# Optimization experiments

Hardware: AMD Instinct MI355X
Metric: run time of the kernel (lower is better)

## Reference

```python
import jax, jax.numpy as jnp
import numpy as np

DIM = 768
HEADS = 16
DIM_HEAD = DIM // HEADS
SCALE = DIM_HEAD ** -0.5


def setup_inputs() -> dict:
    key = jax.random.key(0)
    k1, k2, k3, k4 = jax.random.split(key, 4)
    B, N = 8, 1024
    x = jax.random.normal(k1, (B, N, DIM), dtype=jnp.float32)
    # nn.Linear(dim, 3*dim, bias=False): stored so that qkv = x @ Wqkv
    Wqkv = jax.random.normal(k2, (DIM, 3 * DIM), dtype=jnp.float32) * (DIM ** -0.5)
    Wo = jax.random.normal(k3, (DIM, DIM), dtype=jnp.float32) * (DIM ** -0.5)
    bo = jax.random.normal(k4, (DIM,), dtype=jnp.float32) * 0.01
    return {"x": x, "Wqkv": Wqkv, "Wo": Wo, "bo": bo}


def reference(x, Wqkv, Wo, bo):
    B, N, _ = x.shape
    qkv = x @ Wqkv                                   # [B, N, 3*dim]
    # Faithful to torch: qkv.view(3, B, h, N, dim_head) — raw memory reshape
    qkv = jnp.reshape(qkv, (3, B, HEADS, N, DIM_HEAD))
    q, k, v = qkv[0], qkv[1], qkv[2]                 # each [B, h, N, dh]
    attn = jnp.einsum('bhnd,bhmd->bhnm', q, k) * SCALE   # [B, h, N, N]
    weight = jax.nn.softmax(attn, axis=-1)
    context = jnp.einsum('bhnm,bhmd->bhnd', weight, v)   # [B, h, N, dh]
    # Faithful to torch: context.view(B, -1, dim) — raw memory reshape
    concat = jnp.reshape(context, (B, N, DIM))
    return concat @ Wo + bo                          # dropout is identity at eval
```

## Files before the change

### kernel.cpp

```cpp
#include <hip/hip_runtime.h>
#include <hip/hip_bf16.h>

typedef __bf16 bf16x8 __attribute__((ext_vector_type(8)));
typedef __bf16 bf16x4 __attribute__((ext_vector_type(4)));
typedef float  f32x4  __attribute__((ext_vector_type(4)));

#define C2LOG 0.20823509f

__device__ __forceinline__ void gload_lds16(const __bf16* g, __bf16* l) {
    __builtin_amdgcn_global_load_lds(
        (const __attribute__((address_space(1))) void*)g,
        (__attribute__((address_space(3))) void*)l,
        16, 0, 0);
}

__global__ void cvt_f32_bf16_kernel(const float* __restrict__ in, __bf16* __restrict__ out, int n) {
    int i = (blockIdx.x * blockDim.x + threadIdx.x) * 4;
    if (i < n) {
        float4 v = *(const float4*)&in[i];
        bf16x4 o;
        o[0] = (__bf16)v.x; o[1] = (__bf16)v.y; o[2] = (__bf16)v.z; o[3] = (__bf16)v.w;
        *(bf16x4*)&out[i] = o;
    }
}

__global__ void transpose_f32_bf16_kernel(const float* __restrict__ in, __bf16* __restrict__ out,
                                          int R, int C) {
    __shared__ float tile[32][33];
    int c0 = blockIdx.x * 32, r0 = blockIdx.y * 32;
    int tx = threadIdx.x, ty = threadIdx.y;
#pragma unroll
    for (int i = 0; i < 4; ++i)
        tile[ty + i * 8][tx] = in[(size_t)(r0 + ty + i * 8) * C + c0 + tx];
    __syncthreads();
#pragma unroll
    for (int i = 0; i < 4; ++i)
        out[(size_t)(c0 + ty + i * 8) * R + r0 + tx] = (__bf16)tile[tx][ty + i * 8];
}

template <bool BF16_OUT>
__global__ __launch_bounds__(256, 2)
void gemm_bt_kernel(const __bf16* __restrict__ A, const __bf16* __restrict__ B,
                    void* __restrict__ C, const float* __restrict__ bias,
                    int M, int N, int K) {
    __shared__ __bf16 sA[128 * 32];
    __shared__ __bf16 sB[128 * 32];

    const int m0 = blockIdx.y * 128;
    const int n0 = blockIdx.x * 128;
    const int t = threadIdx.x;
    const int w = t >> 6, lane = t & 63;
    const int quad = lane >> 4, l15 = lane & 15;
    const int wm = w >> 1, wn = w & 1;

    f32x4 acc[4][4] = {};

    for (int k0 = 0; k0 < K; k0 += 32) {
#pragma unroll
        for (int half = 0; half < 2; ++half) {
            const int row = half * 64 + w * 16 + (lane >> 2);
            const int kk = k0 + (lane & 3) * 8;
            gload_lds16(A + (size_t)(m0 + row) * K + kk, &sA[half * 2048 + w * 512]);
            gload_lds16(B + (size_t)(n0 + row) * K + kk, &sB[half * 2048 + w * 512]);
        }
        __syncthreads();

        bf16x8 aF[4], bF[4];
#pragma unroll
        for (int mt = 0; mt < 4; ++mt)
            aF[mt] = *(const bf16x8*)&sA[(wm * 64 + mt * 16 + l15) * 32 + quad * 8];
#pragma unroll
        for (int nt = 0; nt < 4; ++nt)
            bF[nt] = *(const bf16x8*)&sB[(wn * 64 + nt * 16 + l15) * 32 + quad * 8];
#pragma unroll
        for (int mt = 0; mt < 4; ++mt)
#pragma unroll
            for (int nt = 0; nt < 4; ++nt)
                acc[mt][nt] = __builtin_amdgcn_mfma_f32_16x16x32_bf16(aF[mt], bF[nt], acc[mt][nt], 0, 0, 0);
        __syncthreads();
    }

#pragma unroll
    for (int nt = 0; nt < 4; ++nt) {
        const int col = n0 + wn * 64 + nt * 16 + l15;
        float bv = 0.f;
        if (!BF16_OUT) bv = bias[col];
#pragma unroll
        for (int mt = 0; mt < 4; ++mt) {
#pragma unroll
            for (int r = 0; r < 4; ++r) {
                const int row = m0 + wm * 64 + mt * 16 + quad * 4 + r;
                if (BF16_OUT)
                    ((__bf16*)C)[(size_t)row * N + col] = (__bf16)acc[mt][nt][r];
                else
                    ((float*)C)[(size_t)row * N + col] = acc[mt][nt][r] + bv;
            }
        }
    }
}

#define VT_STRIDE 132
#define P_STRIDE  132

__global__ __launch_bounds__(512, 4)
void attn_kernel(const __bf16* __restrict__ Y1, __bf16* __restrict__ Ctx) {
    __shared__ __bf16 Kl[128 * 64];
    __shared__ __bf16 Vt[48 * VT_STRIDE];
    __shared__ __bf16 Pl[128 * P_STRIDE];

    const int bx = blockIdx.x;
    const int bh = bx & 127, qt = bx >> 7;
    const int t = threadIdx.x, w = t >> 6, lane = t & 63;
    const int quad = lane >> 4, l15 = lane & 15;

    const size_t qBase = (size_t)bh * 49152;
    const size_t kBase = 6291456 + qBase;
    const size_t vBase = 12582912 + qBase;

    bf16x8 qf0, qf1;
    {
        const int row = qt * 128 + w * 16 + l15;
        qf0 = *(const bf16x8*)(Y1 + qBase + (size_t)row * 48 + quad * 8);
        if (quad < 2)
            qf1 = *(const bf16x8*)(Y1 + qBase + (size_t)row * 48 + 32 + quad * 8);
        else
            qf1 = bf16x8{};
    }

    const int ku0 = t, ku1 = t + 512;
    const int kr0 = ku0 >> 3, kd0 = ku0 & 7;
    const int kr1 = ku1 >> 3, kd1 = ku1 & 7;
    int vkp[3], vdb[3], vkk[3];
#pragma unroll
    for (int c = 0; c < 3; ++c) {
        const int u = t + c * 512;
        vkp[c] = u & 127;
        vdb[c] = (u >> 7) * 4;
        vkk[c] = (vkp[c] >> 3) + ((vkp[c] & 7) << 4);
    }

    bf16x8 kreg0 = *(const bf16x8*)(Y1 + kBase + (size_t)kr0 * 48 + kd0 * 8);
    bf16x8 kreg1 = *(const bf16x8*)(Y1 + kBase + (size_t)kr1 * 48 + kd1 * 8);
    bf16x4 vreg[3];
#pragma unroll
    for (int c = 0; c < 3; ++c)
        vreg[c] = *(const bf16x4*)(Y1 + vBase + (size_t)vkk[c] * 48 + vdb[c]);

    f32x4 o[3] = {};
    float l_lane[4] = {0.f, 0.f, 0.f, 0.f};

    for (int it = 0; it < 8; ++it) {
        __syncthreads();

        *(bf16x8*)&Kl[kr0 * 64 + ((kd0 ^ (kr0 & 7)) << 3)] = kreg0;
        *(bf16x8*)&Kl[kr1 * 64 + ((kd1 ^ (kr1 & 7)) << 3)] = kreg1;
#pragma unroll
        for (int c = 0; c < 3; ++c)
#pragma unroll
            for (int j = 0; j < 4; ++j)
                Vt[(vdb[c] + j) * VT_STRIDE + vkp[c]] = vreg[c][j];

        if (it < 7) {
            const int kv1 = (it + 1) * 128;
            kreg0 = *(const bf16x8*)(Y1 + kBase + (size_t)(kv1 + kr0) * 48 + kd0 * 8);
            kreg1 = *(const bf16x8*)(Y1 + kBase + (size_t)(kv1 + kr1) * 48 + kd1 * 8);
#pragma unroll
            for (int c = 0; c < 3; ++c)
                vreg[c] = *(const bf16x4*)(Y1 + vBase + (size_t)(kv1 + vkk[c]) * 48 + vdb[c]);
        }

        __syncthreads();

        f32x4 s[8];
#pragma unroll
        for (int nt = 0; nt < 8; ++nt) {
            const int krow = nt * 16 + l15;
            const int base = krow * 64;
            bf16x8 kf0 = *(const bf16x8*)&Kl[base + ((quad ^ (krow & 7)) << 3)];
            bf16x8 kf1 = *(const bf16x8*)&Kl[base + (((4 + quad) ^ (krow & 7)) << 3)];
            f32x4 z = {};
            z = __builtin_amdgcn_mfma_f32_16x16x32_bf16(qf0, kf0, z, 0, 0, 0);
            s[nt] = __builtin_amdgcn_mfma_f32_16x16x32_bf16(qf1, kf1, z, 0, 0, 0);
        }

#pragma unroll
        for (int r = 0; r < 4; ++r) {
            bf16x8 pk;
            float ls = 0.f;
#pragma unroll
            for (int nt = 0; nt < 8; ++nt) {
                float p = __builtin_amdgcn_exp2f(s[nt][r] * C2LOG);
                ls += p;
                pk[nt] = (__bf16)p;
            }
            l_lane[r] += ls;
            *(bf16x8*)&Pl[(w * 16 + quad * 4 + r) * P_STRIDE + l15 * 8] = pk;
        }

        bf16x8 pa[4];
#pragma unroll
        for (int ks = 0; ks < 4; ++ks)
            pa[ks] = *(const bf16x8*)&Pl[(w * 16 + l15) * P_STRIDE + ks * 32 + quad * 8];
#pragma unroll
        for (int nt = 0; nt < 3; ++nt) {
#pragma unroll
            for (int ks = 0; ks < 4; ++ks) {
                bf16x8 vb = *(const bf16x8*)&Vt[(nt * 16 + l15) * VT_STRIDE + ks * 32 + quad * 8];
                o[nt] = __builtin_amdgcn_mfma_f32_16x16x32_bf16(pa[ks], vb, o[nt], 0, 0, 0);
            }
        }
    }

    float inv[4];
#pragma unroll
    for (int r = 0; r < 4; ++r) {
        float ls = l_lane[r];
#pragma unroll
        for (int off = 1; off < 16; off <<= 1)
            ls += __shfl_xor(ls, off);
        inv[r] = __builtin_amdgcn_rcpf(ls);
    }

    __syncthreads();
    __bf16* Ob = Vt;
#pragma unroll
    for (int nt = 0; nt < 3; ++nt) {
        const int d = nt * 16 + l15;
#pragma unroll
        for (int r = 0; r < 4; ++r)
            Ob[(w * 16 + quad * 4 + r) * 48 + d] = (__bf16)(o[nt][r] * inv[r]);
    }
    __syncthreads();
    __bf16* dst = Ctx + qBase + (size_t)qt * 128 * 48;
    *(bf16x8*)(dst + t * 8) = *(const bf16x8*)&Ob[t * 8];
    if (t < 256)
        *(bf16x8*)(dst + (t + 512) * 8) = *(const bf16x8*)&Ob[(t + 512) * 8];
}

extern "C" void kernel_launch(void* const* d_in, const int* in_sizes, int n_in,
                              void* d_out, int out_size, void* d_ws, size_t ws_size,
                              hipStream_t stream) {
    const float* x    = (const float*)d_in[0];
    const float* Wqkv = (const float*)d_in[1];
    const float* Wo   = (const float*)d_in[2];
    const float* bo   = (const float*)d_in[3];
    float* out = (float*)d_out;

    char* ws = (char*)d_ws;
    __bf16* Xbf    = (__bf16*)(ws + 0);
    __bf16* WqkvT  = (__bf16*)(ws + 12582912);
    __bf16* WoT    = (__bf16*)(ws + 16121856);
    __bf16* Y1     = (__bf16*)(ws + 17301504);
    __bf16* Ctx    = (__bf16*)(ws + 55050240);

    cvt_f32_bf16_kernel<<<6144, 256, 0, stream>>>(x, Xbf, 8192 * 768);
    transpose_f32_bf16_kernel<<<dim3(72, 24), dim3(32, 8), 0, stream>>>(Wqkv, WqkvT, 768, 2304);
    transpose_f32_bf16_kernel<<<dim3(24, 24), dim3(32, 8), 0, stream>>>(Wo, WoT, 768, 768);

    gemm_bt_kernel<true><<<dim3(18, 64), 256, 0, stream>>>(Xbf, WqkvT, Y1, nullptr, 8192, 2304, 768);

    attn_kernel<<<1024, 512, 0, stream>>>(Y1, Ctx);

    gemm_bt_kernel<false><<<dim3(6, 64), 256, 0, stream>>>(Ctx, WoT, out, bo, 8192, 768, 768);
}
```

Before: 210.3 us.

## Fuse prepass kernels, split attention KV across warps, narrower output GEMM tiles

Merges the fp32-to-bf16 conversion and both weight transposes into one prepass launch to cut launch overhead. The attention kernel now has each warp cover 32 query rows and half of each 128-key tile, with partial outputs and row sums combined through shared memory at the end. The softmax scale is folded into Q during the load, and the V prefetch permutation is changed to match. The output projection uses a new 128x64-tile GEMM with launch bounds raised to 4, giving more blocks on the 768-wide output. Costs are an extra cross-warp reduction, another barrier, and slightly less accurate bf16 rounding of the pre-scaled Q.

```diff
diff --git a/kernel.cpp b/kernel.cpp
--- a/kernel.cpp
+++ b/kernel.cpp
@@ -14,35 +14,47 @@
         16, 0, 0);
 }
 
-__global__ void cvt_f32_bf16_kernel(const float* __restrict__ in, __bf16* __restrict__ out, int n) {
-    int i = (blockIdx.x * blockDim.x + threadIdx.x) * 4;
-    if (i < n) {
-        float4 v = *(const float4*)&in[i];
+__global__ __launch_bounds__(256)
+void prepass_kernel(const float* __restrict__ x, const float* __restrict__ Wqkv,
+                    const float* __restrict__ Wo, __bf16* __restrict__ Xbf,
+                    __bf16* __restrict__ WqkvT, __bf16* __restrict__ WoT) {
+    __shared__ float tile[32][33];
+    const int bx = blockIdx.x, t = threadIdx.x;
+    if (bx < 6144) {
+        const int i = (bx * 256 + t) * 4;
+        float4 v = *(const float4*)&x[i];
         bf16x4 o;
         o[0] = (__bf16)v.x; o[1] = (__bf16)v.y; o[2] = (__bf16)v.z; o[3] = (__bf16)v.w;
-        *(bf16x4*)&out[i] = o;
-    }
-}
-
-__global__ void transpose_f32_bf16_kernel(const float* __restrict__ in, __bf16* __restrict__ out,
-                                          int R, int C) {
-    __shared__ float tile[32][33];
-    int c0 = blockIdx.x * 32, r0 = blockIdx.y * 32;
-    int tx = threadIdx.x, ty = threadIdx.y;
-#pragma unroll
-    for (int i = 0; i < 4; ++i)
-        tile[ty + i * 8][tx] = in[(size_t)(r0 + ty + i * 8) * C + c0 + tx];
-    __syncthreads();
-#pragma unroll
-    for (int i = 0; i < 4; ++i)
-        out[(size_t)(c0 + ty + i * 8) * R + r0 + tx] = (__bf16)tile[tx][ty + i * 8];
-}
-
-template <bool BF16_OUT>
+        *(bf16x4*)&Xbf[i] = o;
+        return;
+    }
+    const float* in; __bf16* out; int R, C, bxx;
+    if (bx < 6144 + 1728) { bxx = bx - 6144; in = Wqkv; out = WqkvT; R = 768; C = 2304;
+        const int c0 = (bxx % 72) * 32, r0 = (bxx / 72) * 32;
+        const int tx = t & 31, ty = t >> 5;
+#pragma unroll
+        for (int i = 0; i < 4; ++i)
+            tile[ty + i * 8][tx] = in[(size_t)(r0 + ty + i * 8) * C + c0 + tx];
+        __syncthreads();
+#pragma unroll
+        for (int i = 0; i < 4; ++i)
+            out[(size_t)(c0 + ty + i * 8) * R + r0 + tx] = (__bf16)tile[tx][ty + i * 8];
+    } else { bxx = bx - 6144 - 1728; in = Wo; out = WoT; R = 768; C = 768;
+        const int c0 = (bxx % 24) * 32, r0 = (bxx / 24) * 32;
+        const int tx = t & 31, ty = t >> 5;
+#pragma unroll
+        for (int i = 0; i < 4; ++i)
+            tile[ty + i * 8][tx] = in[(size_t)(r0 + ty + i * 8) * C + c0 + tx];
+        __syncthreads();
+#pragma unroll
+        for (int i = 0; i < 4; ++i)
+            out[(size_t)(c0 + ty + i * 8) * R + r0 + tx] = (__bf16)tile[tx][ty + i * 8];
+    }
+}
+
 __global__ __launch_bounds__(256, 2)
 void gemm_bt_kernel(const __bf16* __restrict__ A, const __bf16* __restrict__ B,
-                    void* __restrict__ C, const float* __restrict__ bias,
-                    int M, int N, int K) {
+                    __bf16* __restrict__ C, int M, int N, int K) {
     __shared__ __bf16 sA[128 * 32];
     __shared__ __bf16 sB[128 * 32];
 
@@ -83,60 +95,123 @@
 #pragma unroll
     for (int nt = 0; nt < 4; ++nt) {
         const int col = n0 + wn * 64 + nt * 16 + l15;
-        float bv = 0.f;
-        if (!BF16_OUT) bv = bias[col];
-#pragma unroll
-        for (int mt = 0; mt < 4; ++mt) {
+#pragma unroll
+        for (int mt = 0; mt < 4; ++mt)
 #pragma unroll
             for (int r = 0; r < 4; ++r) {
                 const int row = m0 + wm * 64 + mt * 16 + quad * 4 + r;
-                if (BF16_OUT)
-                    ((__bf16*)C)[(size_t)row * N + col] = (__bf16)acc[mt][nt][r];
-                else
-                    ((float*)C)[(size_t)row * N + col] = acc[mt][nt][r] + bv;
-            }
-        }
+                C[(size_t)row * N + col] = (__bf16)acc[mt][nt][r];
+            }
+    }
+}
+
+__global__ __launch_bounds__(256, 4)
+void gemm_bt64_kernel(const __bf16* __restrict__ A, const __bf16* __restrict__ B,
+                      float* __restrict__ C, const float* __restrict__ bias,
+                      int M, int N, int K) {
+    __shared__ __bf16 sA[128 * 32];
+    __shared__ __bf16 sB[64 * 32];
+
+    const int m0 = blockIdx.y * 128;
+    const int n0 = blockIdx.x * 64;
+    const int t = threadIdx.x;
+    const int w = t >> 6, lane = t & 63;
+    const int quad = lane >> 4, l15 = lane & 15;
+
+    f32x4 acc[2][4] = {};
+
+    for (int k0 = 0; k0 < K; k0 += 32) {
+        const int kk = k0 + (lane & 3) * 8;
+#pragma unroll
+        for (int p = 0; p < 2; ++p) {
+            const int row = w * 32 + p * 16 + (lane >> 2);
+            gload_lds16(A + (size_t)(m0 + row) * K + kk, &sA[w * 1024 + p * 512]);
+        }
+        {
+            const int row = w * 16 + (lane >> 2);
+            gload_lds16(B + (size_t)(n0 + row) * K + kk, &sB[w * 512]);
+        }
+        __syncthreads();
+
+        bf16x8 aF[2], bF[4];
+#pragma unroll
+        for (int mt = 0; mt < 2; ++mt)
+            aF[mt] = *(const bf16x8*)&sA[(w * 32 + mt * 16 + l15) * 32 + quad * 8];
+#pragma unroll
+        for (int nt = 0; nt < 4; ++nt)
+            bF[nt] = *(const bf16x8*)&sB[(nt * 16 + l15) * 32 + quad * 8];
+#pragma unroll
+        for (int mt = 0; mt < 2; ++mt)
+#pragma unroll
+            for (int nt = 0; nt < 4; ++nt)
+                acc[mt][nt] = __builtin_amdgcn_mfma_f32_16x16x32_bf16(aF[mt], bF[nt], acc[mt][nt], 0, 0, 0);
+        __syncthreads();
+    }
+
+#pragma unroll
+    for (int nt = 0; nt < 4; ++nt) {
+        const int col = n0 + nt * 16 + l15;
+        const float bv = bias[col];
+#pragma unroll
+        for (int mt = 0; mt < 2; ++mt)
+#pragma unroll
+            for (int r = 0; r < 4; ++r) {
+                const int row = m0 + w * 32 + mt * 16 + quad * 4 + r;
+                C[(size_t)row * N + col] = acc[mt][nt][r] + bv;
+            }
     }
 }
 
 #define VT_STRIDE 132
 #define P_STRIDE  132
+#define KL_ELEMS  (128 * 64)
+#define VT_ELEMS  (48 * VT_STRIDE)
 
 __global__ __launch_bounds__(512, 4)
 void attn_kernel(const __bf16* __restrict__ Y1, __bf16* __restrict__ Ctx) {
-    __shared__ __bf16 Kl[128 * 64];
-    __shared__ __bf16 Vt[48 * VT_STRIDE];
-    __shared__ __bf16 Pl[128 * P_STRIDE];
+    __shared__ __bf16 smem[KL_ELEMS + VT_ELEMS + 128 * P_STRIDE];
+    __bf16* Kl = smem;
+    __bf16* Vt = smem + KL_ELEMS;
+    __bf16* Pl = Vt + VT_ELEMS;
+    float*  Red = (float*)smem;
+    __bf16* Ob  = Pl;
 
     const int bx = blockIdx.x;
     const int bh = bx & 127, qt = bx >> 7;
     const int t = threadIdx.x, w = t >> 6, lane = t & 63;
     const int quad = lane >> 4, l15 = lane & 15;
+    const int wq = w & 3, kh = w >> 2;
+    const int khb = kh * 64;
 
     const size_t qBase = (size_t)bh * 49152;
     const size_t kBase = 6291456 + qBase;
     const size_t vBase = 12582912 + qBase;
 
-    bf16x8 qf0, qf1;
-    {
-        const int row = qt * 128 + w * 16 + l15;
-        qf0 = *(const bf16x8*)(Y1 + qBase + (size_t)row * 48 + quad * 8);
-        if (quad < 2)
-            qf1 = *(const bf16x8*)(Y1 + qBase + (size_t)row * 48 + 32 + quad * 8);
-        else
-            qf1 = bf16x8{};
-    }
-
-    const int ku0 = t, ku1 = t + 512;
-    const int kr0 = ku0 >> 3, kd0 = ku0 & 7;
-    const int kr1 = ku1 >> 3, kd1 = ku1 & 7;
+    bf16x8 qfA[2], qfB[2];
+#pragma unroll
+    for (int mt = 0; mt < 2; ++mt) {
+        const int row = qt * 128 + wq * 32 + mt * 16 + l15;
+        bf16x8 a = *(const bf16x8*)(Y1 + qBase + (size_t)row * 48 + quad * 8);
+#pragma unroll
+        for (int j = 0; j < 8; ++j) a[j] = (__bf16)((float)a[j] * C2LOG);
+        qfA[mt] = a;
+        if (quad < 2) {
+            bf16x8 b = *(const bf16x8*)(Y1 + qBase + (size_t)row * 48 + 32 + quad * 8);
+#pragma unroll
+            for (int j = 0; j < 8; ++j) b[j] = (__bf16)((float)b[j] * C2LOG);
+            qfB[mt] = b;
+        } else qfB[mt] = bf16x8{};
+    }
+
+    const int kr0 = t >> 3, kd0 = t & 7;
+    const int kr1 = (t + 512) >> 3, kd1 = (t + 512) & 7;
     int vkp[3], vdb[3], vkk[3];
 #pragma unroll
     for (int c = 0; c < 3; ++c) {
         const int u = t + c * 512;
         vkp[c] = u & 127;
         vdb[c] = (u >> 7) * 4;
-        vkk[c] = (vkp[c] >> 3) + ((vkp[c] & 7) << 4);
+        vkk[c] = (vkp[c] >> 6) * 64 + (vkp[c] & 3) * 16 + ((vkp[c] >> 2) & 15);
     }
 
     bf16x8 kreg0 = *(const bf16x8*)(Y1 + kBase + (size_t)kr0 * 48 + kd0 * 8);
@@ -146,8 +221,8 @@
     for (int c = 0; c < 3; ++c)
         vreg[c] = *(const bf16x4*)(Y1 + vBase + (size_t)vkk[c] * 48 + vdb[c]);
 
-    f32x4 o[3] = {};
-    float l_lane[4] = {0.f, 0.f, 0.f, 0.f};
+    f32x4 o[2][3] = {};
+    float l_lane[2][4] = {};
 
     for (int it = 0; it < 8; ++it) {
         __syncthreads();
@@ -171,66 +246,111 @@
 
         __syncthreads();
 
-        f32x4 s[8];
-#pragma unroll
-        for (int nt = 0; nt < 8; ++nt) {
-            const int krow = nt * 16 + l15;
+        f32x4 s[2][4];
+#pragma unroll
+        for (int nt = 0; nt < 4; ++nt) {
+            const int krow = khb + nt * 16 + l15;
             const int base = krow * 64;
             bf16x8 kf0 = *(const bf16x8*)&Kl[base + ((quad ^ (krow & 7)) << 3)];
             bf16x8 kf1 = *(const bf16x8*)&Kl[base + (((4 + quad) ^ (krow & 7)) << 3)];
-            f32x4 z = {};
-            z = __builtin_amdgcn_mfma_f32_16x16x32_bf16(qf0, kf0, z, 0, 0, 0);
-            s[nt] = __builtin_amdgcn_mfma_f32_16x16x32_bf16(qf1, kf1, z, 0, 0, 0);
-        }
-
+#pragma unroll
+            for (int mt = 0; mt < 2; ++mt) {
+                f32x4 z = {};
+                z = __builtin_amdgcn_mfma_f32_16x16x32_bf16(qfA[mt], kf0, z, 0, 0, 0);
+                s[mt][nt] = __builtin_amdgcn_mfma_f32_16x16x32_bf16(qfB[mt], kf1, z, 0, 0, 0);
+            }
+        }
+
+#pragma unroll
+        for (int mt = 0; mt < 2; ++mt)
+#pragma unroll
+            for (int r = 0; r < 4; ++r) {
+                bf16x4 pk;
+                float ls = 0.f;
+#pragma unroll
+                for (int nt = 0; nt < 4; ++nt) {
+                    float p = __builtin_amdgcn_exp2f(s[mt][nt][r]);
+                    ls += p;
+                    pk[nt] = (__bf16)p;
+                }
+                l_lane[mt][r] += ls;
+                const int row = wq * 32 + mt * 16 + quad * 4 + r;
+                *(bf16x4*)&Pl[row * P_STRIDE + khb + l15 * 4] = pk;
+            }
+
+        bf16x8 pa[2][2];
+#pragma unroll
+        for (int mt = 0; mt < 2; ++mt)
+#pragma unroll
+            for (int ks = 0; ks < 2; ++ks)
+                pa[mt][ks] = *(const bf16x8*)&Pl[(wq * 32 + mt * 16 + l15) * P_STRIDE + khb + ks * 32 + quad * 8];
+#pragma unroll
+        for (int nd = 0; nd < 3; ++nd)
+#pragma unroll
+            for (int ks = 0; ks < 2; ++ks) {
+                bf16x8 vb = *(const bf16x8*)&Vt[(nd * 16 + l15) * VT_STRIDE + khb + ks * 32 + quad * 8];
+#pragma unroll
+                for (int mt = 0; mt < 2; ++mt)
+                    o[mt][nd] = __builtin_amdgcn_mfma_f32_16x16x32_bf16(pa[mt][ks], vb, o[mt][nd], 0, 0, 0);
+            }
+    }
+
+    float lr[2][4];
+#pragma unroll
+    for (int mt = 0; mt < 2; ++mt)
 #pragma unroll
         for (int r = 0; r < 4; ++r) {
-            bf16x8 pk;
-            float ls = 0.f;
-#pragma unroll
-            for (int nt = 0; nt < 8; ++nt) {
-                float p = __builtin_amdgcn_exp2f(s[nt][r] * C2LOG);
-                ls += p;
-                pk[nt] = (__bf16)p;
-            }
-            l_lane[r] += ls;
-            *(bf16x8*)&Pl[(w * 16 + quad * 4 + r) * P_STRIDE + l15 * 8] = pk;
-        }
-
-        bf16x8 pa[4];
-#pragma unroll
-        for (int ks = 0; ks < 4; ++ks)
-            pa[ks] = *(const bf16x8*)&Pl[(w * 16 + l15) * P_STRIDE + ks * 32 + quad * 8];
-#pragma unroll
-        for (int nt = 0; nt < 3; ++nt) {
-#pragma unroll
-            for (int ks = 0; ks < 4; ++ks) {
-                bf16x8 vb = *(const bf16x8*)&Vt[(nt * 16 + l15) * VT_STRIDE + ks * 32 + quad * 8];
-                o[nt] = __builtin_amdgcn_mfma_f32_16x16x32_bf16(pa[ks], vb, o[nt], 0, 0, 0);
-            }
-        }
-    }
-
-    float inv[4];
-#pragma unroll
-    for (int r = 0; r < 4; ++r) {
-        float ls = l_lane[r];
-#pragma unroll
-        for (int off = 1; off < 16; off <<= 1)
-            ls += __shfl_xor(ls, off);
-        inv[r] = __builtin_amdgcn_rcpf(ls);
-    }
+            float ls = l_lane[mt][r];
+#pragma unroll
+            for (int off = 1; off < 16; off <<= 1)
+                ls += __shfl_xor(ls, off);
+            lr[mt][r] = ls;
+        }
 
     __syncthreads();
-    __bf16* Ob = Vt;
-#pragma unroll
-    for (int nt = 0; nt < 3; ++nt) {
-        const int d = nt * 16 + l15;
-#pragma unroll
-        for (int r = 0; r < 4; ++r)
-            Ob[(w * 16 + quad * 4 + r) * 48 + d] = (__bf16)(o[nt][r] * inv[r]);
+
+    if (kh == 1) {
+#pragma unroll
+        for (int mt = 0; mt < 2; ++mt) {
+#pragma unroll
+            for (int nd = 0; nd < 3; ++nd) {
+                const int d = nd * 16 + l15;
+#pragma unroll
+                for (int r = 0; r < 4; ++r) {
+                    const int row = wq * 32 + mt * 16 + quad * 4 + r;
+                    Red[row * 49 + d] = o[mt][nd][r];
+                }
+            }
+            if (l15 == 0)
+#pragma unroll
+                for (int r = 0; r < 4; ++r)
+                    Red[(wq * 32 + mt * 16 + quad * 4 + r) * 49 + 48] = lr[mt][r];
+        }
     }
     __syncthreads();
+
+    if (kh == 0) {
+#pragma unroll
+        for (int mt = 0; mt < 2; ++mt) {
+            float inv[4];
+#pragma unroll
+            for (int r = 0; r < 4; ++r) {
+                const int row = wq * 32 + mt * 16 + quad * 4 + r;
+                inv[r] = __builtin_amdgcn_rcpf(lr[mt][r] + Red[row * 49 + 48]);
+            }
+#pragma unroll
+            for (int nd = 0; nd < 3; ++nd) {
+                const int d = nd * 16 + l15;
+#pragma unroll
+                for (int r = 0; r < 4; ++r) {
+                    const int row = wq * 32 + mt * 16 + quad * 4 + r;
+                    Ob[row * 48 + d] = (__bf16)((o[mt][nd][r] + Red[row * 49 + d]) * inv[r]);
+                }
+            }
+        }
+    }
+    __syncthreads();
+
     __bf16* dst = Ctx + qBase + (size_t)qt * 128 * 48;
     *(bf16x8*)(dst + t * 8) = *(const bf16x8*)&Ob[t * 8];
     if (t < 256)
@@ -253,13 +373,11 @@
     __bf16* Y1     = (__bf16*)(ws + 17301504);
     __bf16* Ctx    = (__bf16*)(ws + 55050240);
 
-    cvt_f32_bf16_kernel<<<6144, 256, 0, stream>>>(x, Xbf, 8192 * 768);
-    transpose_f32_bf16_kernel<<<dim3(72, 24), dim3(32, 8), 0, stream>>>(Wqkv, WqkvT, 768, 2304);
-    transpose_f32_bf16_kernel<<<dim3(24, 24), dim3(32, 8), 0, stream>>>(Wo, WoT, 768, 768);
-
-    gemm_bt_kernel<true><<<dim3(18, 64), 256, 0, stream>>>(Xbf, WqkvT, Y1, nullptr, 8192, 2304, 768);
+    prepass_kernel<<<8448, 256, 0, stream>>>(x, Wqkv, Wo, Xbf, WqkvT, WoT);
+
+    gemm_bt_kernel<<<dim3(18, 64), 256, 0, stream>>>(Xbf, WqkvT, Y1, 8192, 2304, 768);
 
     attn_kernel<<<1024, 512, 0, stream>>>(Y1, Ctx);
 
-    gemm_bt_kernel<false><<<dim3(6, 64), 256, 0, stream>>>(Ctx, WoT, out, bo, 8192, 768, 768);
-}
+    gemm_bt64_kernel<<<dim3(12, 64), 256, 0, stream>>>(Ctx, WoT, out, bo, 8192, 768, 768);
+}
```

Measured after the change: 256.2 us. 21.9% more time.

## Merge prepass kernels, add 128x64 output GEMM, raise QKV GEMM occupancy

Applied to the files above, without the earlier changes.

Folds the x conversion and the two weight transposes into one prepass launch to cut launch overhead. Adds a 128x64-tile GEMM for the output projection so it runs 768 blocks instead of 384, filling more compute units on a small-N problem. Raises the launch-bounds occupancy hint on the QKV GEMM from 2 to 3 blocks per SM, which may constrain registers. The attention index change is cosmetic.

```diff
diff --git a/kernel.cpp b/kernel.cpp
--- a/kernel.cpp
+++ b/kernel.cpp
@@ -14,35 +14,47 @@
         16, 0, 0);
 }
 
-__global__ void cvt_f32_bf16_kernel(const float* __restrict__ in, __bf16* __restrict__ out, int n) {
-    int i = (blockIdx.x * blockDim.x + threadIdx.x) * 4;
-    if (i < n) {
-        float4 v = *(const float4*)&in[i];
+__global__ __launch_bounds__(256)
+void prepass_kernel(const float* __restrict__ x, const float* __restrict__ Wqkv,
+                    const float* __restrict__ Wo, __bf16* __restrict__ Xbf,
+                    __bf16* __restrict__ WqkvT, __bf16* __restrict__ WoT) {
+    __shared__ float tile[32][33];
+    const int bx = blockIdx.x, t = threadIdx.x;
+    if (bx < 6144) {
+        const int i = (bx * 256 + t) * 4;
+        float4 v = *(const float4*)&x[i];
         bf16x4 o;
         o[0] = (__bf16)v.x; o[1] = (__bf16)v.y; o[2] = (__bf16)v.z; o[3] = (__bf16)v.w;
-        *(bf16x4*)&out[i] = o;
-    }
-}
-
-__global__ void transpose_f32_bf16_kernel(const float* __restrict__ in, __bf16* __restrict__ out,
-                                          int R, int C) {
-    __shared__ float tile[32][33];
-    int c0 = blockIdx.x * 32, r0 = blockIdx.y * 32;
-    int tx = threadIdx.x, ty = threadIdx.y;
-#pragma unroll
-    for (int i = 0; i < 4; ++i)
-        tile[ty + i * 8][tx] = in[(size_t)(r0 + ty + i * 8) * C + c0 + tx];
-    __syncthreads();
-#pragma unroll
-    for (int i = 0; i < 4; ++i)
-        out[(size_t)(c0 + ty + i * 8) * R + r0 + tx] = (__bf16)tile[tx][ty + i * 8];
-}
-
-template <bool BF16_OUT>
-__global__ __launch_bounds__(256, 2)
+        *(bf16x4*)&Xbf[i] = o;
+        return;
+    }
+    const float* in; __bf16* out; int R, C, bxx;
+    if (bx < 6144 + 1728) { bxx = bx - 6144; in = Wqkv; out = WqkvT; R = 768; C = 2304;
+        const int c0 = (bxx % 72) * 32, r0 = (bxx / 72) * 32;
+        const int tx = t & 31, ty = t >> 5;
+#pragma unroll
+        for (int i = 0; i < 4; ++i)
+            tile[ty + i * 8][tx] = in[(size_t)(r0 + ty + i * 8) * C + c0 + tx];
+        __syncthreads();
+#pragma unroll
+        for (int i = 0; i < 4; ++i)
+            out[(size_t)(c0 + ty + i * 8) * R + r0 + tx] = (__bf16)tile[tx][ty + i * 8];
+    } else { bxx = bx - 6144 - 1728; in = Wo; out = WoT; R = 768; C = 768;
+        const int c0 = (bxx % 24) * 32, r0 = (bxx / 24) * 32;
+        const int tx = t & 31, ty = t >> 5;
+#pragma unroll
+        for (int i = 0; i < 4; ++i)
+            tile[ty + i * 8][tx] = in[(size_t)(r0 + ty + i * 8) * C + c0 + tx];
+        __syncthreads();
+#pragma unroll
+        for (int i = 0; i < 4; ++i)
+            out[(size_t)(c0 + ty + i * 8) * R + r0 + tx] = (__bf16)tile[tx][ty + i * 8];
+    }
+}
+
+__global__ __launch_bounds__(256, 3)
 void gemm_bt_kernel(const __bf16* __restrict__ A, const __bf16* __restrict__ B,
-                    void* __restrict__ C, const float* __restrict__ bias,
-                    int M, int N, int K) {
+                    __bf16* __restrict__ C, int M, int N, int K) {
     __shared__ __bf16 sA[128 * 32];
     __shared__ __bf16 sB[128 * 32];
 
@@ -83,19 +95,70 @@
 #pragma unroll
     for (int nt = 0; nt < 4; ++nt) {
         const int col = n0 + wn * 64 + nt * 16 + l15;
-        float bv = 0.f;
-        if (!BF16_OUT) bv = bias[col];
-#pragma unroll
-        for (int mt = 0; mt < 4; ++mt) {
+#pragma unroll
+        for (int mt = 0; mt < 4; ++mt)
 #pragma unroll
             for (int r = 0; r < 4; ++r) {
                 const int row = m0 + wm * 64 + mt * 16 + quad * 4 + r;
-                if (BF16_OUT)
-                    ((__bf16*)C)[(size_t)row * N + col] = (__bf16)acc[mt][nt][r];
-                else
-                    ((float*)C)[(size_t)row * N + col] = acc[mt][nt][r] + bv;
+                C[(size_t)row * N + col] = (__bf16)acc[mt][nt][r];
             }
-        }
+    }
+}
+
+__global__ __launch_bounds__(256, 4)
+void gemm_bt64_kernel(const __bf16* __restrict__ A, const __bf16* __restrict__ B,
+                      float* __restrict__ C, const float* __restrict__ bias,
+                      int M, int N, int K) {
+    __shared__ __bf16 sA[128 * 32];
+    __shared__ __bf16 sB[64 * 32];
+
+    const int m0 = blockIdx.y * 128;
+    const int n0 = blockIdx.x * 64;
+    const int t = threadIdx.x;
+    const int w = t >> 6, lane = t & 63;
+    const int quad = lane >> 4, l15 = lane & 15;
+
+    f32x4 acc[2][4] = {};
+
+    for (int k0 = 0; k0 < K; k0 += 32) {
+        const int kk = k0 + (lane & 3) * 8;
+#pragma unroll
+        for (int p = 0; p < 2; ++p) {
+            const int row = w * 32 + p * 16 + (lane >> 2);
+            gload_lds16(A + (size_t)(m0 + row) * K + kk, &sA[w * 1024 + p * 512]);
+        }
+        {
+            const int row = w * 16 + (lane >> 2);
+            gload_lds16(B + (size_t)(n0 + row) * K + kk, &sB[w * 512]);
+        }
+        __syncthreads();
+
+        bf16x8 aF[2], bF[4];
+#pragma unroll
+        for (int mt = 0; mt < 2; ++mt)
+            aF[mt] = *(const bf16x8*)&sA[(w * 32 + mt * 16 + l15) * 32 + quad * 8];
+#pragma unroll
+        for (int nt = 0; nt < 4; ++nt)
+            bF[nt] = *(const bf16x8*)&sB[(nt * 16 + l15) * 32 + quad * 8];
+#pragma unroll
+        for (int mt = 0; mt < 2; ++mt)
+#pragma unroll
+            for (int nt = 0; nt < 4; ++nt)
+                acc[mt][nt] = __builtin_amdgcn_mfma_f32_16x16x32_bf16(aF[mt], bF[nt], acc[mt][nt], 0, 0, 0);
+        __syncthreads();
+    }
+
+#pragma unroll
+    for (int nt = 0; nt < 4; ++nt) {
+        const int col = n0 + nt * 16 + l15;
+        const float bv = bias[col];
+#pragma unroll
+        for (int mt = 0; mt < 2; ++mt)
+#pragma unroll
+            for (int r = 0; r < 4; ++r) {
+                const int row = m0 + w * 32 + mt * 16 + quad * 4 + r;
+                C[(size_t)row * N + col] = acc[mt][nt][r] + bv;
+            }
     }
 }
 
@@ -127,9 +190,8 @@
             qf1 = bf16x8{};
     }
 
-    const int ku0 = t, ku1 = t + 512;
-    const int kr0 = ku0 >> 3, kd0 = ku0 & 7;
-    const int kr1 = ku1 >> 3, kd1 = ku1 & 7;
+    const int kr0 = t >> 3, kd0 = t & 7;
+    const int kr1 = (t + 512) >> 3, kd1 = (t + 512) & 7;
     int vkp[3], vdb[3], vkk[3];
 #pragma unroll
     for (int c = 0; c < 3; ++c) {
@@ -253,13 +315,11 @@
     __bf16* Y1     = (__bf16*)(ws + 17301504);
     __bf16* Ctx    = (__bf16*)(ws + 55050240);
 
-    cvt_f32_bf16_kernel<<<6144, 256, 0, stream>>>(x, Xbf, 8192 * 768);
-    transpose_f32_bf16_kernel<<<dim3(72, 24), dim3(32, 8), 0, stream>>>(Wqkv, WqkvT, 768, 2304);
-    transpose_f32_bf16_kernel<<<dim3(24, 24), dim3(32, 8), 0, stream>>>(Wo, WoT, 768, 768);
-
-    gemm_bt_kernel<true><<<dim3(18, 64), 256, 0, stream>>>(Xbf, WqkvT, Y1, nullptr, 8192, 2304, 768);
+    prepass_kernel<<<8448, 256, 0, stream>>>(x, Wqkv, Wo, Xbf, WqkvT, WoT);
+
+    gemm_bt_kernel<<<dim3(18, 64), 256, 0, stream>>>(Xbf, WqkvT, Y1, 8192, 2304, 768);
 
     attn_kernel<<<1024, 512, 0, stream>>>(Y1, Ctx);
 
-    gemm_bt_kernel<false><<<dim3(6, 64), 256, 0, stream>>>(Ctx, WoT, out, bo, 8192, 768, 768);
-}
+    gemm_bt64_kernel<<<dim3(12, 64), 256, 0, stream>>>(Ctx, WoT, out, bo, 8192, 768, 768);
+}
```

Result: faster. 205.2 us (-2.4%).
